# Kernel optimization log

Hardware: AMD Instinct MI355X
Metric: run time of the kernel (lower is better)

Reference implementation:

```python
import jax, jax.numpy as jnp
import numpy as np

VOXEL_SIZE = 0.01  # sparse_model.pres


def setup_inputs() -> dict:
    key = jax.random.key(0)
    k1, k2, k3 = jax.random.split(key, 3)
    B, N, F = 32, 262144, 3
    x = jax.random.normal(k1, (B, N, F), dtype=jnp.float32)
    W = jax.random.normal(k2, (F, F), dtype=jnp.float32) * 0.5  # stand-in diff_unet weight
    b = jax.random.normal(k3, (F,), dtype=jnp.float32) * 0.1    # stand-in diff_unet bias
    return {"x": x, "W": W, "b": b}


def reference(x, W, b):
    # x: [B, N, F] point cloud
    B, N, F = x.shape
    P = B * N
    # _quantize: shift coords to be non-negative per cloud, then voxelize
    coords = x - jnp.min(x, axis=1, keepdims=True)          # [B, N, F]
    vox = jnp.floor(coords / VOXEL_SIZE).astype(jnp.int32)  # integer voxel coords
    vflat = vox.reshape(P, F)
    bidx = jnp.broadcast_to(jnp.arange(B, dtype=jnp.int32)[:, None], (B, N)).reshape(P)
    # batch_sparse_quantize orders points by (batch, voxel-hash); with a fine
    # voxel grid every point is a unique voxel, so `indices` is the full
    # permutation given by a stable lexicographic sort of the voxel keys.
    indices = jnp.lexsort((vflat[:, 2], vflat[:, 1], vflat[:, 0], bidx)).astype(jnp.int32)
    # inverse_indices[indices] = arange  (scatter-based permutation inversion)
    inverse = jnp.zeros_like(indices).at[indices].set(jnp.arange(P, dtype=jnp.int32))
    # fancy-indexed gather of features
    feats = x.reshape(P, F)[indices]                        # [P, F]
    # stand-in for diff_unet: per-point affine map
    out_feats = feats @ W + b                               # [P, F]
    # _inverse_quantize: scatter back to original point order
    return out_feats[inverse].reshape(B, N, F)
```

## Files before the change

### kernel.cpp

```cpp
#include <hip/hip_runtime.h>


typedef float f32x4 __attribute__((ext_vector_type(4)));

constexpr int TPB = 256;
constexpr int TILE_F4 = TPB * 3;

__global__ __launch_bounds__(TPB) void affine3_kernel(
    const float* __restrict__ x,
    const float* __restrict__ W,
    const float* __restrict__ bias,
    float* __restrict__ out,
    long long ntiles,
    long long npoints)
{
    __shared__ f32x4 lds[TILE_F4];

    const float w00 = W[0], w01 = W[1], w02 = W[2];
    const float w10 = W[3], w11 = W[4], w12 = W[5];
    const float w20 = W[6], w21 = W[7], w22 = W[8];
    const float b0 = bias[0], b1 = bias[1], b2 = bias[2];

    const int t = threadIdx.x;
    const f32x4* __restrict__ xin = reinterpret_cast<const f32x4*>(x);
    f32x4* __restrict__ xout      = reinterpret_cast<f32x4*>(out);

    for (long long tile = blockIdx.x; tile < ntiles; tile += gridDim.x) {
        const long long base = tile * TILE_F4;

        f32x4 v0 = xin[base + 3 * t + 0];
        f32x4 v1 = xin[base + 3 * t + 1];
        f32x4 v2 = xin[base + 3 * t + 2];

        float p0x = v0.x, p0y = v0.y, p0z = v0.z;
        float p1x = v0.w, p1y = v1.x, p1z = v1.y;
        float p2x = v1.z, p2y = v1.w, p2z = v2.x;
        float p3x = v2.y, p3y = v2.z, p3z = v2.w;

        float o0x = fmaf(p0x, w00, fmaf(p0y, w10, fmaf(p0z, w20, b0)));
        float o0y = fmaf(p0x, w01, fmaf(p0y, w11, fmaf(p0z, w21, b1)));
        float o0z = fmaf(p0x, w02, fmaf(p0y, w12, fmaf(p0z, w22, b2)));

        float o1x = fmaf(p1x, w00, fmaf(p1y, w10, fmaf(p1z, w20, b0)));
        float o1y = fmaf(p1x, w01, fmaf(p1y, w11, fmaf(p1z, w21, b1)));
        float o1z = fmaf(p1x, w02, fmaf(p1y, w12, fmaf(p1z, w22, b2)));

        float o2x = fmaf(p2x, w00, fmaf(p2y, w10, fmaf(p2z, w20, b0)));
        float o2y = fmaf(p2x, w01, fmaf(p2y, w11, fmaf(p2z, w21, b1)));
        float o2z = fmaf(p2x, w02, fmaf(p2y, w12, fmaf(p2z, w22, b2)));

        float o3x = fmaf(p3x, w00, fmaf(p3y, w10, fmaf(p3z, w20, b0)));
        float o3y = fmaf(p3x, w01, fmaf(p3y, w11, fmaf(p3z, w21, b1)));
        float o3z = fmaf(p3x, w02, fmaf(p3y, w12, fmaf(p3z, w22, b2)));

        lds[3 * t + 0] = f32x4{o0x, o0y, o0z, o1x};
        lds[3 * t + 1] = f32x4{o1y, o1z, o2x, o2y};
        lds[3 * t + 2] = f32x4{o2z, o3x, o3y, o3z};

        __syncthreads();

        f32x4 s0 = lds[t];
        f32x4 s1 = lds[TPB + t];
        f32x4 s2 = lds[2 * TPB + t];
        __builtin_nontemporal_store(s0, &xout[base + t]);
        __builtin_nontemporal_store(s1, &xout[base + TPB + t]);
        __builtin_nontemporal_store(s2, &xout[base + 2 * TPB + t]);

        __syncthreads();
    }

    const long long donePts = ntiles * (TILE_F4 * 4LL / 3LL);
    for (long long p = donePts + (long long)blockIdx.x * TPB + t;
         p < npoints; p += (long long)gridDim.x * TPB) {
        float px = x[p * 3 + 0], py = x[p * 3 + 1], pz = x[p * 3 + 2];
        out[p * 3 + 0] = fmaf(px, w00, fmaf(py, w10, fmaf(pz, w20, b0)));
        out[p * 3 + 1] = fmaf(px, w01, fmaf(py, w11, fmaf(pz, w21, b1)));
        out[p * 3 + 2] = fmaf(px, w02, fmaf(py, w12, fmaf(pz, w22, b2)));
    }
}

extern "C" void kernel_launch(void* const* d_in, const int* in_sizes, int n_in,
                              void* d_out, int out_size, void* d_ws, size_t ws_size,
                              hipStream_t stream) {
    const float* x    = (const float*)d_in[0];
    const float* W    = (const float*)d_in[1];
    const float* bias = (const float*)d_in[2];
    float* out        = (float*)d_out;

    const long long n       = (long long)in_sizes[0];
    const long long npoints = n / 3;
    const long long totalF4 = n / 4;
    const long long ntiles  = totalF4 / TILE_F4;

    long long want = ntiles < 2048 ? (ntiles > 0 ? ntiles : 1) : 2048;
    int grid = (int)want;

    affine3_kernel<<<grid, TPB, 0, stream>>>(x, W, bias, out, ntiles, npoints);
}
```

Baseline: 35.04 us.

## Stage loads through swizzled LDS and launch one block per tile

Global loads become fully coalesced (each thread reads consecutive float4s across the block) and are staged through a swizzled LDS buffer before the per-thread point regrouping. Output staging uses a second swizzled buffer to avoid bank conflicts. The grid-stride loop is replaced with one tile per block, so the grid grows to ntiles (about 8192) instead of being capped at 2048. This adds one extra LDS round trip and barrier per tile, and drops the loop's reuse of each block across tiles.

```diff
diff --git a/kernel.cpp b/kernel.cpp
--- a/kernel.cpp
+++ b/kernel.cpp
@@ -5,6 +5,8 @@
 
 constexpr int TPB = 256;
 constexpr int TILE_F4 = TPB * 3;
+
+#define SWZ(s) ((s) ^ ((((s) >> 3)) & 7))
 
 __global__ __launch_bounds__(TPB) void affine3_kernel(
     const float* __restrict__ x,
@@ -14,7 +16,8 @@
     long long ntiles,
     long long npoints)
 {
-    __shared__ f32x4 lds[TILE_F4];
+    __shared__ f32x4 A[TILE_F4];
+    __shared__ f32x4 B[TILE_F4];
 
     const float w00 = W[0], w01 = W[1], w02 = W[2];
     const float w10 = W[3], w11 = W[4], w12 = W[5];
@@ -25,12 +28,20 @@
     const f32x4* __restrict__ xin = reinterpret_cast<const f32x4*>(x);
     f32x4* __restrict__ xout      = reinterpret_cast<f32x4*>(out);
 
-    for (long long tile = blockIdx.x; tile < ntiles; tile += gridDim.x) {
+    const long long tile = blockIdx.x;
+    if (tile < ntiles) {
         const long long base = tile * TILE_F4;
 
-        f32x4 v0 = xin[base + 3 * t + 0];
-        f32x4 v1 = xin[base + 3 * t + 1];
-        f32x4 v2 = xin[base + 3 * t + 2];
+        #pragma unroll
+        for (int i = 0; i < 3; ++i) {
+            const int s = i * TPB + t;
+            A[SWZ(s)] = xin[base + s];
+        }
+        __syncthreads();
+
+        f32x4 v0 = A[SWZ(3 * t + 0)];
+        f32x4 v1 = A[SWZ(3 * t + 1)];
+        f32x4 v2 = A[SWZ(3 * t + 2)];
 
         float p0x = v0.x, p0y = v0.y, p0z = v0.z;
         float p1x = v0.w, p1y = v1.x, p1z = v1.y;
@@ -53,25 +64,22 @@
         float o3y = fmaf(p3x, w01, fmaf(p3y, w11, fmaf(p3z, w21, b1)));
         float o3z = fmaf(p3x, w02, fmaf(p3y, w12, fmaf(p3z, w22, b2)));
 
-        lds[3 * t + 0] = f32x4{o0x, o0y, o0z, o1x};
-        lds[3 * t + 1] = f32x4{o1y, o1z, o2x, o2y};
-        lds[3 * t + 2] = f32x4{o2z, o3x, o3y, o3z};
-
+        B[SWZ(3 * t + 0)] = f32x4{o0x, o0y, o0z, o1x};
+        B[SWZ(3 * t + 1)] = f32x4{o1y, o1z, o2x, o2y};
+        B[SWZ(3 * t + 2)] = f32x4{o2z, o3x, o3y, o3z};
         __syncthreads();
 
-        f32x4 s0 = lds[t];
-        f32x4 s1 = lds[TPB + t];
-        f32x4 s2 = lds[2 * TPB + t];
-        __builtin_nontemporal_store(s0, &xout[base + t]);
-        __builtin_nontemporal_store(s1, &xout[base + TPB + t]);
-        __builtin_nontemporal_store(s2, &xout[base + 2 * TPB + t]);
-
-        __syncthreads();
+        #pragma unroll
+        for (int i = 0; i < 3; ++i) {
+            const int s = i * TPB + t;
+            __builtin_nontemporal_store(B[SWZ(s)], &xout[base + s]);
+        }
     }
 
-    const long long donePts = ntiles * (TILE_F4 * 4LL / 3LL);
-    for (long long p = donePts + (long long)blockIdx.x * TPB + t;
-         p < npoints; p += (long long)gridDim.x * TPB) {
+    const long long donePts = ntiles * 1024;
+    const long long gtid    = (long long)blockIdx.x * TPB + t;
+    const long long gstride = (long long)gridDim.x * TPB;
+    for (long long p = donePts + gtid; p < npoints; p += gstride) {
         float px = x[p * 3 + 0], py = x[p * 3 + 1], pz = x[p * 3 + 2];
         out[p * 3 + 0] = fmaf(px, w00, fmaf(py, w10, fmaf(pz, w20, b0)));
         out[p * 3 + 1] = fmaf(px, w01, fmaf(py, w11, fmaf(pz, w21, b1)));
@@ -92,8 +100,7 @@
     const long long totalF4 = n / 4;
     const long long ntiles  = totalF4 / TILE_F4;
 
-    long long want = ntiles < 2048 ? (ntiles > 0 ? ntiles : 1) : 2048;
-    int grid = (int)want;
+    long long grid = ntiles > 0 ? ntiles : 1;
 
-    affine3_kernel<<<grid, TPB, 0, stream>>>(x, W, bias, out, ntiles, npoints);
+    affine3_kernel<<<(int)grid, TPB, 0, stream>>>(x, W, bias, out, ntiles, npoints);
 }
```

New measurement: 34.06 us. 1.03x faster.
